# Performance work log

Hardware: AMD Instinct MI355X
Metric: run time of the kernel (lower is better)

## Reference

```python
import jax, jax.numpy as jnp
import numpy as np
from functools import lru_cache
from jax.scipy.linalg import expm

N_QUBITS = 6
DIM = 2 ** N_QUBITS          # 64
N_PAULI = 4 ** N_QUBITS      # 4096


@lru_cache(maxsize=None)
def _pauli_tensor_np(n_qubits):
    # All n-qubit Pauli strings as dense matrices, ordered base-4
    # (digit 0..3 -> I, X, Y, Z; most-significant digit = first qubit).
    I = np.eye(2, dtype=np.complex64)
    X = np.array([[0, 1], [1, 0]], dtype=np.complex64)
    Y = np.array([[0, -1j], [1j, 0]], dtype=np.complex64)
    Z = np.array([[1, 0], [0, -1]], dtype=np.complex64)
    base = np.stack([I, X, Y, Z])  # [4,2,2]
    T = base
    for _ in range(n_qubits - 1):
        k, d = T.shape[0], T.shape[1]
        T = np.einsum('iab,jcd->ijacbd', T, base).reshape(k * 4, d * 2, d * 2)
    return np.ascontiguousarray(T.astype(np.complex64))  # [4^n, 2^n, 2^n]


def setup_inputs() -> dict:
    key = jax.random.key(0)
    kx, kw, kb = jax.random.split(key, 3)
    x = jax.random.normal(kx, (512, 4000), dtype=jnp.float32)
    weight = jax.random.normal(kw, (4, N_PAULI - 1), dtype=jnp.float32)
    bias = jax.random.normal(kb, (DIM,), dtype=jnp.float32)
    return {"x": x, "weight": weight, "bias": bias}


def reference(x, weight, bias):
    # x: [B, in_dim] float32; weight: [n_reps, 4^n - 1]; bias: [out_dim]
    B, in_dim = x.shape
    n_reps = weight.shape[0]
    out_dim = bias.shape[0]
    P = jnp.asarray(_pauli_tensor_np(N_QUBITS))  # [4096, 64, 64] complex64

    # Pad data coefficients up to the full Pauli basis (identity included).
    xp = jnp.pad(x, ((0, 0), (0, N_PAULI - in_dim))).astype(jnp.complex64)

    # Data-encoding Hamiltonian per sample: H_d[b] = sum_p x[b,p] * P[p]
    Hd = jnp.einsum('bp,pij->bij', xp, P)                       # [B,64,64]
    Ud = jax.vmap(expm)(-1j * Hd)                               # [B,64,64]

    # Trainable Hamiltonians per rep (identity Pauli excluded -> global phase).
    Hp = jnp.einsum('rp,pij->rij', weight.astype(jnp.complex64), P[1:])
    Up = jax.vmap(expm)(-1j * Hp)                               # [R,64,64]

    # Data re-uploading circuit on |0...0>: repeat (U_param @ U_data).
    psi = jnp.zeros((B, DIM), dtype=jnp.complex64).at[:, 0].set(1.0)
    for r in range(n_reps):
        psi = jnp.einsum('bij,bj->bi', Ud, psi)
        psi = jnp.einsum('ij,bj->bi', Up[r], psi)

    # Observables are computational-basis projectors |k><k|, k < out_dim:
    # <psi|O_k|psi> = |psi_k|^2
    probs = (psi[:, :out_dim].real ** 2 + psi[:, :out_dim].imag ** 2)
    return probs.astype(jnp.float32) + bias
```

## Files before the change

### kernel.cpp

```cpp
#include <hip/hip_runtime.h>
#include <math.h>

typedef float2 cplx;
typedef __attribute__((ext_vector_type(8))) short short8v;
typedef __attribute__((ext_vector_type(4))) short short4v;
typedef __attribute__((ext_vector_type(4))) float float4v;

#define TPB 256
#define IN_DIM 4000
#define NREPS 4

#define C0f  1.0f
#define C1f  1.0f
#define C2f  0.5f
#define C3f  0.16666667f
#define C4f  0.041666668f
#define C5f  8.3333333e-3f
#define C6f  1.3888889e-3f
#define C7f  1.9841270e-4f
#define C8f  2.4801587e-5f
#define C9f  2.7557319e-6f
#define C10f 2.7557319e-7f
#define C11f 2.5052108e-8f
#define C12f 2.0876757e-9f
#define C13f 1.6059044e-10f
#define C14f 1.1470746e-11f
#define C15f 7.6471637e-13f

#define MFMA(A,B,C) __builtin_amdgcn_mfma_f32_16x16x32_bf16((A),(B),(C),0,0,0)


__device__ __forceinline__ int idxSw(int a, int b) {
    return (a << 6) + ((((b >> 3) + a) & 7) << 3) + (b & 7);
}
__device__ __forceinline__ short f2bf(float f) {
    unsigned u = __float_as_uint(f);
    return (short)((u + 0x7FFF + ((u >> 16) & 1)) >> 16);
}
__device__ __forceinline__ float bf2f(short s) {
    return __uint_as_float(((unsigned)(unsigned short)s) << 16);
}
__device__ __forceinline__ short8v neg8(short8v a) {
    int4 u; __builtin_memcpy(&u, &a, 16);
    u.x ^= 0x80008000; u.y ^= 0x80008000; u.z ^= 0x80008000; u.w ^= 0x80008000;
    short8v r; __builtin_memcpy(&r, &u, 16); return r;
}

template<int AM, int BM>
__device__ __forceinline__ void mm_mfma(const short* __restrict__ As,
                                        const short* __restrict__ Bs,
                                        int li, int q, int mh, int nh,
                                        float4v* __restrict__ accR,
                                        float4v* __restrict__ accI)
{
    #pragma unroll
    for (int ks = 0; ks < 2; ks++) {
        const int ch = ks * 4 + q;
        short8v arh[2], arl[2], cRh[2], cRl[2], cIh[2], cIl[2];
        #pragma unroll
        for (int dm = 0; dm < 2; dm++) {
            int r = ((mh * 2 + dm) << 4) + li;
            int off = (r << 6) + (((ch + r) & 7) << 3);
            arh[dm] = *(const short8v*)(As + off);
            arl[dm] = *(const short8v*)(As + 4096 + off);
            short8v aih = *(const short8v*)(As + 8192 + off);
            short8v ail = *(const short8v*)(As + 12288 + off);
            short8v nih = neg8(aih), nil_ = neg8(ail);
            cRh[dm] = (AM == 2) ? aih : nih;
            cRl[dm] = (AM == 2) ? ail : nil_;
            cIh[dm] = (AM == 2) ? nih : aih;
            cIl[dm] = (AM == 2) ? nil_ : ail;
        }
        #pragma unroll
        for (int dn = 0; dn < 2; dn++) {
            int n = ((nh * 2 + dn) << 4) + li;
            int off = (n << 6) + (((ch + n) & 7) << 3);
            short8v brh = *(const short8v*)(Bs + off);
            short8v brl = *(const short8v*)(Bs + 4096 + off);
            short8v bih = *(const short8v*)(Bs + 8192 + off);
            short8v bil = *(const short8v*)(Bs + 12288 + off);
            if (BM == 1) { brh = neg8(brh); brl = neg8(brl); }
            #pragma unroll
            for (int dm = 0; dm < 2; dm++) {
                int ti = dm * 2 + dn;
                accR[ti] = MFMA(arh[dm], brh, accR[ti]);
                accR[ti] = MFMA(arh[dm], brl, accR[ti]);
                accR[ti] = MFMA(arl[dm], brh, accR[ti]);
                accR[ti] = MFMA(cRh[dm], bih, accR[ti]);
                accR[ti] = MFMA(cRh[dm], bil, accR[ti]);
                accR[ti] = MFMA(cRl[dm], bih, accR[ti]);
                accI[ti] = MFMA(arh[dm], bih, accI[ti]);
                accI[ti] = MFMA(arh[dm], bil, accI[ti]);
                accI[ti] = MFMA(arl[dm], bih, accI[ti]);
                accI[ti] = MFMA(cIh[dm], brh, accI[ti]);
                accI[ti] = MFMA(cIh[dm], brl, accI[ti]);
                accI[ti] = MFMA(cIl[dm], brh, accI[ti]);
            }
        }
    }
}

__device__ __forceinline__ void write_row(short* __restrict__ S, int li, int q,
                                          int mh, int nh,
                                          const float4v* cre, const float4v* cim)
{
    #pragma unroll
    for (int dm = 0; dm < 2; dm++)
    #pragma unroll
    for (int dn = 0; dn < 2; dn++) {
        int ti = dm * 2 + dn;
        int c = ((nh * 2 + dn) << 4) + li;
        #pragma unroll
        for (int reg = 0; reg < 4; reg++) {
            int r = ((mh * 2 + dm) << 4) + q * 4 + reg;
            int off = idxSw(r, c);
            float vr = cre[ti][reg], vi = cim[ti][reg];
            short rh = f2bf(vr), rl = f2bf(vr - bf2f(rh));
            short ih = f2bf(vi), il = f2bf(vi - bf2f(ih));
            S[off] = rh; S[4096 + off] = rl; S[8192 + off] = ih; S[12288 + off] = il;
        }
    }
}

__device__ __forceinline__ void write_rowT(short* __restrict__ S, int li, int q,
                                           int mh, int nh,
                                           const float4v* cre, const float4v* cim)
{
    #pragma unroll
    for (int dm = 0; dm < 2; dm++)
    #pragma unroll
    for (int dn = 0; dn < 2; dn++) {
        int ti = dm * 2 + dn;
        int c = ((nh * 2 + dn) << 4) + li;
        int k0 = ((mh * 2 + dm) << 4) + q * 4;
        int off = idxSw(c, k0);
        short4v rh, rl, ih, il;
        #pragma unroll
        for (int reg = 0; reg < 4; reg++) {
            float vr = cre[ti][reg], vi = cim[ti][reg];
            short h1 = f2bf(vr); rh[reg] = h1; rl[reg] = f2bf(vr - bf2f(h1));
            short h2 = f2bf(vi); ih[reg] = h2; il[reg] = f2bf(vi - bf2f(h2));
        }
        *(short4v*)(S + off) = rh;
        *(short4v*)(S + 4096 + off) = rl;
        *(short4v*)(S + 8192 + off) = ih;
        *(short4v*)(S + 12288 + off) = il;
    }
}

__device__ __forceinline__ void gather_tile(const short* __restrict__ S, int li, int q,
                                            int mh, int nh, float4v* bre, float4v* bim)
{
    #pragma unroll
    for (int dm = 0; dm < 2; dm++)
    #pragma unroll
    for (int dn = 0; dn < 2; dn++) {
        int ti = dm * 2 + dn;
        int c = ((nh * 2 + dn) << 4) + li;
        #pragma unroll
        for (int reg = 0; reg < 4; reg++) {
            int r = ((mh * 2 + dm) << 4) + q * 4 + reg;
            int off = idxSw(r, c);
            bre[ti][reg] = bf2f(S[off]) + bf2f(S[4096 + off]);
            bim[ti][reg] = bf2f(S[8192 + off]) + bf2f(S[12288 + off]);
        }
    }
}

__device__ __forceinline__ void adddiag(float4v* ure, float cI, int li, int q, int mh, int nh)
{
    #pragma unroll
    for (int dm = 0; dm < 2; dm++)
    #pragma unroll
    for (int dn = 0; dn < 2; dn++) {
        if (2 * mh + dm == 2 * nh + dn) {
            #pragma unroll
            for (int e = 0; e < 4; e++)
                if (li == q * 4 + e) ure[dm * 2 + dn][e] += cI;
        }
    }
}

__device__ __forceinline__ void pauli_masks(int p, int& xm, int& zm) {
    xm = 0; zm = 0;
    #pragma unroll
    for (int k = 0; k < 6; k++) {
        int lo = (p >> (2 * k)) & 1;
        int hi = (p >> (2 * k + 1)) & 1;
        zm |= hi << k;
        xm |= (hi ^ lo) << k;
    }
}
__device__ __forceinline__ cplx pauli_phase(float v, int xm, int zm) {
    int ny = __popc(xm & zm) & 3;
    if (ny == 0) return make_float2(v, 0.f);
    if (ny == 1) return make_float2(0.f, -v);
    if (ny == 2) return make_float2(-v, 0.f);
    return make_float2(0.f, v);
}

__device__ __forceinline__ void expm_core(char* __restrict__ LDS,
                                          const float* __restrict__ src, bool isW,
                                          int t, float4v* ure, float4v* uim)
{
    short* S0 = (short*)LDS;
    short* S1 = (short*)(LDS + 32768);
    cplx*  W  = (cplx*)(LDS + 32768);
    float* red = (float*)(LDS + 65536);
    const int lane = t & 63, wv = t >> 6;

    float sumsq = 0.f;
    #pragma unroll
    for (int n = 0; n < 16; n++) {
        int p = t + TPB * n;
        float v = isW ? ((p == 0) ? 0.f : src[p - 1])
                      : ((p < IN_DIM) ? src[p] : 0.f);
        sumsq += v * v;
        int xm, zm; pauli_masks(p, xm, zm);
        W[(xm << 6) + zm] = pauli_phase(v, xm, zm);
    }
    #pragma unroll
    for (int d = 32; d >= 1; d >>= 1) sumsq += __shfl_xor(sumsq, d, 64);
    if (lane == 0) red[wv] = sumsq;
    __syncthreads();

    float fro = sqrtf(64.f * (red[0] + red[1] + red[2] + red[3]));
    int s1 = 0; { float nn = fro; while (nn > 8.f && s1 < 24) { nn *= 0.5f; s1++; } }
    float sc1 = exp2f((float)(-s1));

    cplx hv[16];
    #pragma unroll
    for (int rr = 0; rr < 16; rr++) hv[rr] = W[(((wv << 4) + rr) << 6) + lane];
    #pragma unroll
    for (int d = 1; d < 64; d <<= 1) {
        float sg = (lane & d) ? -1.f : 1.f;
        #pragma unroll
        for (int rr = 0; rr < 16; rr++) {
            float px = __shfl_xor(hv[rr].x, d, 64);
            float py = __shfl_xor(hv[rr].y, d, 64);
            hv[rr].x = fmaf(sg, hv[rr].x, px);
            hv[rr].y = fmaf(sg, hv[rr].y, py);
        }
    }
    __syncthreads();

    #pragma unroll
    for (int rr = 0; rr < 16; rr++) {
        int m = (wv << 4) + rr;
        int c = lane ^ m;
        float vr = hv[rr].y * sc1, vi = -hv[rr].x * sc1;
        short rh = f2bf(vr), rl = f2bf(vr - bf2f(rh));
        short ih = f2bf(vi), il = f2bf(vi - bf2f(ih));
        int off = idxSw(lane, c);
        S0[off] = rh; S0[4096 + off] = rl; S0[8192 + off] = ih; S0[12288 + off] = il;
    }
    __syncthreads();

    const int li = lane & 15, q = lane >> 4;
    const int mh = wv & 1, nh = wv >> 1;
    const float4v z4 = {0.f, 0.f, 0.f, 0.f};
    float4v accR[4], accI[4];
    #define ZERO_ACC _Pragma("unroll") for (int i2 = 0; i2 < 4; i2++) { accR[i2]=z4; accI[i2]=z4; }

    ZERO_ACC
    mm_mfma<0, 1>(S0, S0, li, q, mh, nh, accR, accI);
    float ss = 0.f;
    #pragma unroll
    for (int ti = 0; ti < 4; ti++)
        #pragma unroll
        for (int e = 0; e < 4; e++)
            ss += accR[ti][e]*accR[ti][e] + accI[ti][e]*accI[ti][e];
    #pragma unroll
    for (int d = 32; d >= 1; d >>= 1) ss += __shfl_xor(ss, d, 64);
    if (lane == 0) red[4 + wv] = ss;
    __syncthreads();

    float bound = sqrtf(sqrtf(red[4] + red[5] + red[6] + red[7]));
    int ds = 0; { float nn = bound; while (nn > 3.4f && ds < 12) { nn *= 0.5f; ds++; } }
    const int s = s1 + ds;
    float dsc = exp2f((float)(-ds)), dsc2 = dsc * dsc;

    float4v bre[4], bim[4];
    gather_tile(S0, li, q, mh, nh, bre, bim);

    #pragma unroll
    for (int ti = 0; ti < 4; ti++) { ure[ti] = accR[ti] * dsc2; uim[ti] = accI[ti] * dsc2; }
    write_rowT(S1, li, q, mh, nh, ure, uim);
    __syncthreads();

    {
        float ca = C15f * dsc;
        #pragma unroll
        for (int ti = 0; ti < 4; ti++) { ure[ti] = ca * bre[ti]; uim[ti] = ca * bim[ti]; }
        adddiag(ure, C14f, li, q, mh, nh);
        write_rowT(S0, li, q, mh, nh, ure, uim);
    }
    __syncthreads();

    const float cIc[7] = { C0f, C2f, C4f, C6f, C8f, C10f, C12f };
    const float cAc[7] = { C1f, C3f, C5f, C7f, C9f, C11f, C13f };
    for (int j = 6; j >= 0; j--) {
        ZERO_ACC
        mm_mfma<2, 0>(S1, S0, li, q, mh, nh, accR, accI);
        __syncthreads();
        float ca = cAc[j] * dsc, cI = cIc[j];
        #pragma unroll
        for (int ti = 0; ti < 4; ti++) {
            ure[ti] = accR[ti] + ca * bre[ti];
            uim[ti] = accI[ti] + ca * bim[ti];
        }
        adddiag(ure, cI, li, q, mh, nh);
        write_rowT(S0, li, q, mh, nh, ure, uim);
        __syncthreads();
    }

    for (int sq = 0; sq < s; sq++) {
        write_row(S1, li, q, mh, nh, ure, uim);
        if (sq > 0) write_rowT(S0, li, q, mh, nh, ure, uim);
        __syncthreads();
        ZERO_ACC
        mm_mfma<0, 0>(S1, S0, li, q, mh, nh, accR, accI);
        __syncthreads();
        #pragma unroll
        for (int ti = 0; ti < 4; ti++) { ure[ti] = accR[ti]; uim[ti] = accI[ti]; }
    }
    #undef ZERO_ACC
}

__device__ __forceinline__ cplx matvec_partial(const cplx* __restrict__ M,
                                               const cplx* __restrict__ pin,
                                               int i, int g)
{
    float ax = 0.f, ay = 0.f;
    const float4* Mr = (const float4*)(M + (i << 6));
    #pragma unroll
    for (int c = 0; c < 4; c++) {
        int ch = ((g << 2) + c + (i & 15)) & 15;
        int b = (ch >> 2) & 1;
        float4 m01 = Mr[(ch << 1) + b];
        float4 m23 = Mr[(ch << 1) + 1 - b];
        const cplx* p = pin + (ch << 2);
        cplx p0 = p[0], p1 = p[1], p2 = p[2], p3 = p[3];
        ax = fmaf(m01.x, p0.x, fmaf(-m01.y, p0.y, ax));
        ay = fmaf(m01.x, p0.y, fmaf( m01.y, p0.x, ay));
        ax = fmaf(m01.z, p1.x, fmaf(-m01.w, p1.y, ax));
        ay = fmaf(m01.z, p1.y, fmaf( m01.w, p1.x, ay));
        ax = fmaf(m23.x, p2.x, fmaf(-m23.y, p2.y, ax));
        ay = fmaf(m23.x, p2.y, fmaf( m23.y, p2.x, ay));
        ax = fmaf(m23.z, p3.x, fmaf(-m23.w, p3.y, ax));
        ay = fmaf(m23.z, p3.y, fmaf( m23.w, p3.x, ay));
    }
    return make_float2(ax, ay);
}

__global__ __launch_bounds__(TPB) void up_kernel(const float* __restrict__ w,
                                                 cplx* __restrict__ ws)
{
    __shared__ float4 LDSf4[4290];
    char* LDS = (char*)LDSf4;
    const int t = threadIdx.x, r = blockIdx.x;
    float4v ure[4], uim[4];
    expm_core(LDS, w + (size_t)r * 4095, true, t, ure, uim);

    const int lane = t & 63, wv = t >> 6, li = lane & 15, q = lane >> 4;
    const int mh = wv & 1, nh = wv >> 1;
    cplx* dst = ws + ((size_t)r << 12);
    #pragma unroll
    for (int dm = 0; dm < 2; dm++)
    #pragma unroll
    for (int dn = 0; dn < 2; dn++) {
        int ti = dm * 2 + dn;
        int c = ((nh * 2 + dn) << 4) + li;
        int cs = c ^ (((c >> 4) & 1) << 1);
        #pragma unroll
        for (int reg = 0; reg < 4; reg++) {
            int rr = ((mh * 2 + dm) << 4) + q * 4 + reg;
            dst[(rr << 6) + cs] = make_float2(ure[ti][reg], uim[ti][reg]);
        }
    }
}

__global__ __launch_bounds__(TPB) void circuit_kernel(const float* __restrict__ x,
                                                      const cplx* __restrict__ ws,
                                                      const float* __restrict__ bias,
                                                      float* __restrict__ out)
{
    __shared__ float4 LDSf4[4290];
    char* LDS = (char*)LDSf4;
    const int t = threadIdx.x, b = blockIdx.x;
    float4v ure[4], uim[4];
    expm_core(LDS, x + (size_t)b * IN_DIM, false, t, ure, uim);

    cplx* Ud   = (cplx*)(LDS + 32768);
    cplx* UpS  = (cplx*)LDS;
    cplx* psiA = (cplx*)(LDS + 65568);
    cplx* psiB = (cplx*)(LDS + 66080);
    cplx* part = (cplx*)(LDS + 66592);

    const int lane = t & 63, wv = t >> 6, li = lane & 15, q = lane >> 4;
    const int mh = wv & 1, nh = wv >> 1;
    #pragma unroll
    for (int dm = 0; dm < 2; dm++)
    #pragma unroll
    for (int dn = 0; dn < 2; dn++) {
        int ti = dm * 2 + dn;
        int c = ((nh * 2 + dn) << 4) + li;
        int cs = c ^ (((c >> 4) & 1) << 1);
        #pragma unroll
        for (int reg = 0; reg < 4; reg++) {
            int rr = ((mh * 2 + dm) << 4) + q * 4 + reg;
            Ud[(rr << 6) + cs] = make_float2(ure[ti][reg], uim[ti][reg]);
        }
    }
    if (t < 64) psiA[t] = make_float2(t == 0 ? 1.f : 0.f, 0.f);
    __syncthreads();

    const int i = t & 63, g = t >> 6;
    for (int r = 0; r < NREPS; r++) {
        const float4* srcv = (const float4*)(ws + ((size_t)r << 12));
        float4* dstY = (float4*)UpS;
        #pragma unroll
        for (int n = 0; n < 8; n++) dstY[n * TPB + t] = srcv[n * TPB + t];
        __syncthreads();
        part[t] = matvec_partial(Ud, psiA, i, g);
        __syncthreads();
        if (t < 64) {
            cplx a0 = part[t], a1 = part[64 + t], a2 = part[128 + t], a3 = part[192 + t];
            psiB[t] = make_float2(a0.x + a1.x + a2.x + a3.x, a0.y + a1.y + a2.y + a3.y);
        }
        __syncthreads();
        part[t] = matvec_partial(UpS, psiB, i, g);
        __syncthreads();
        if (t < 64) {
            cplx a0 = part[t], a1 = part[64 + t], a2 = part[128 + t], a3 = part[192 + t];
            psiA[t] = make_float2(a0.x + a1.x + a2.x + a3.x, a0.y + a1.y + a2.y + a3.y);
        }
        __syncthreads();
    }
    if (t < 64) {
        cplx pv = psiA[t];
        out[(b << 6) + t] = fmaf(pv.x, pv.x, fmaf(pv.y, pv.y, bias[t]));
    }
}

extern "C" void kernel_launch(void* const* d_in, const int* in_sizes, int n_in,
                              void* d_out, int out_size, void* d_ws, size_t ws_size,
                              hipStream_t stream)
{
    const float* x    = (const float*)d_in[0];
    const float* w    = (const float*)d_in[1];
    const float* bias = (const float*)d_in[2];
    float* out = (float*)d_out;
    cplx* ws   = (cplx*)d_ws;

    int B = in_sizes[0] / IN_DIM;

    hipLaunchKernelGGL(up_kernel,      dim3(NREPS), dim3(TPB), 0, stream, w, ws);
    hipLaunchKernelGGL(circuit_kernel, dim3(B),     dim3(TPB), 0, stream, x, ws, bias, out);
}
```

Before: 166.1 us.

## Template expm core on wave count; use 1024-thread up_kernel and wave-local matvec

Makes the expm routine a template over waves per block, so up_kernel runs with 16 waves (one 16x16 tile per wave) instead of 4, shortening the serial critical path of the 4-block parameter expm. The circuit matvec now has each wave own 16 rows and reduce with shuffles instead of an LDS partial-sum pass, which removes a barrier and a reduction step per half-rep. Pauli mask computation is hoisted out of the load loop and one barrier after the Walsh transform is dropped. Using 1024 threads raises per-block register pressure and barrier cost in up_kernel.

```diff
diff --git a/kernel.cpp b/kernel.cpp
--- a/kernel.cpp
+++ b/kernel.cpp
@@ -6,7 +6,6 @@
 typedef __attribute__((ext_vector_type(4))) short short4v;
 typedef __attribute__((ext_vector_type(4))) float float4v;
 
-#define TPB 256
 #define IN_DIM 4000
 #define NREPS 4
 
@@ -46,20 +45,20 @@
     short8v r; __builtin_memcpy(&r, &u, 16); return r;
 }
 
-template<int AM, int BM>
+template<int AM, int BM, int ND>
 __device__ __forceinline__ void mm_mfma(const short* __restrict__ As,
                                         const short* __restrict__ Bs,
-                                        int li, int q, int mh, int nh,
+                                        int li, int q, int mb, int nb,
                                         float4v* __restrict__ accR,
                                         float4v* __restrict__ accI)
 {
     #pragma unroll
     for (int ks = 0; ks < 2; ks++) {
         const int ch = ks * 4 + q;
-        short8v arh[2], arl[2], cRh[2], cRl[2], cIh[2], cIl[2];
-        #pragma unroll
-        for (int dm = 0; dm < 2; dm++) {
-            int r = ((mh * 2 + dm) << 4) + li;
+        short8v arh[ND], arl[ND], cRh[ND], cRl[ND], cIh[ND], cIl[ND];
+        #pragma unroll
+        for (int dm = 0; dm < ND; dm++) {
+            int r = ((mb + dm) << 4) + li;
             int off = (r << 6) + (((ch + r) & 7) << 3);
             arh[dm] = *(const short8v*)(As + off);
             arl[dm] = *(const short8v*)(As + 4096 + off);
@@ -72,8 +71,8 @@
             cIl[dm] = (AM == 2) ? nil_ : ail;
         }
         #pragma unroll
-        for (int dn = 0; dn < 2; dn++) {
-            int n = ((nh * 2 + dn) << 4) + li;
+        for (int dn = 0; dn < ND; dn++) {
+            int n = ((nb + dn) << 4) + li;
             int off = (n << 6) + (((ch + n) & 7) << 3);
             short8v brh = *(const short8v*)(Bs + off);
             short8v brl = *(const short8v*)(Bs + 4096 + off);
@@ -81,8 +80,8 @@
             short8v bil = *(const short8v*)(Bs + 12288 + off);
             if (BM == 1) { brh = neg8(brh); brl = neg8(brl); }
             #pragma unroll
-            for (int dm = 0; dm < 2; dm++) {
-                int ti = dm * 2 + dn;
+            for (int dm = 0; dm < ND; dm++) {
+                int ti = dm * ND + dn;
                 accR[ti] = MFMA(arh[dm], brh, accR[ti]);
                 accR[ti] = MFMA(arh[dm], brl, accR[ti]);
                 accR[ti] = MFMA(arl[dm], brh, accR[ti]);
@@ -100,19 +99,20 @@
     }
 }
 
+template<int ND>
 __device__ __forceinline__ void write_row(short* __restrict__ S, int li, int q,
-                                          int mh, int nh,
+                                          int mb, int nb,
                                           const float4v* cre, const float4v* cim)
 {
     #pragma unroll
-    for (int dm = 0; dm < 2; dm++)
-    #pragma unroll
-    for (int dn = 0; dn < 2; dn++) {
-        int ti = dm * 2 + dn;
-        int c = ((nh * 2 + dn) << 4) + li;
+    for (int dm = 0; dm < ND; dm++)
+    #pragma unroll
+    for (int dn = 0; dn < ND; dn++) {
+        int ti = dm * ND + dn;
+        int c = ((nb + dn) << 4) + li;
         #pragma unroll
         for (int reg = 0; reg < 4; reg++) {
-            int r = ((mh * 2 + dm) << 4) + q * 4 + reg;
+            int r = ((mb + dm) << 4) + q * 4 + reg;
             int off = idxSw(r, c);
             float vr = cre[ti][reg], vi = cim[ti][reg];
             short rh = f2bf(vr), rl = f2bf(vr - bf2f(rh));
@@ -122,17 +122,18 @@
     }
 }
 
+template<int ND>
 __device__ __forceinline__ void write_rowT(short* __restrict__ S, int li, int q,
-                                           int mh, int nh,
+                                           int mb, int nb,
                                            const float4v* cre, const float4v* cim)
 {
     #pragma unroll
-    for (int dm = 0; dm < 2; dm++)
-    #pragma unroll
-    for (int dn = 0; dn < 2; dn++) {
-        int ti = dm * 2 + dn;
-        int c = ((nh * 2 + dn) << 4) + li;
-        int k0 = ((mh * 2 + dm) << 4) + q * 4;
+    for (int dm = 0; dm < ND; dm++)
+    #pragma unroll
+    for (int dn = 0; dn < ND; dn++) {
+        int ti = dm * ND + dn;
+        int c = ((nb + dn) << 4) + li;
+        int k0 = ((mb + dm) << 4) + q * 4;
         int off = idxSw(c, k0);
         short4v rh, rl, ih, il;
         #pragma unroll
@@ -148,18 +149,19 @@
     }
 }
 
+template<int ND>
 __device__ __forceinline__ void gather_tile(const short* __restrict__ S, int li, int q,
-                                            int mh, int nh, float4v* bre, float4v* bim)
-{
-    #pragma unroll
-    for (int dm = 0; dm < 2; dm++)
-    #pragma unroll
-    for (int dn = 0; dn < 2; dn++) {
-        int ti = dm * 2 + dn;
-        int c = ((nh * 2 + dn) << 4) + li;
+                                            int mb, int nb, float4v* bre, float4v* bim)
+{
+    #pragma unroll
+    for (int dm = 0; dm < ND; dm++)
+    #pragma unroll
+    for (int dn = 0; dn < ND; dn++) {
+        int ti = dm * ND + dn;
+        int c = ((nb + dn) << 4) + li;
         #pragma unroll
         for (int reg = 0; reg < 4; reg++) {
-            int r = ((mh * 2 + dm) << 4) + q * 4 + reg;
+            int r = ((mb + dm) << 4) + q * 4 + reg;
             int off = idxSw(r, c);
             bre[ti][reg] = bf2f(S[off]) + bf2f(S[4096 + off]);
             bim[ti][reg] = bf2f(S[8192 + off]) + bf2f(S[12288 + off]);
@@ -167,30 +169,41 @@
     }
 }
 
-__device__ __forceinline__ void adddiag(float4v* ure, float cI, int li, int q, int mh, int nh)
-{
-    #pragma unroll
-    for (int dm = 0; dm < 2; dm++)
-    #pragma unroll
-    for (int dn = 0; dn < 2; dn++) {
-        if (2 * mh + dm == 2 * nh + dn) {
+template<int ND>
+__device__ __forceinline__ void adddiag(float4v* u, float cI, int li, int q, int mb, int nb)
+{
+    #pragma unroll
+    for (int dm = 0; dm < ND; dm++)
+    #pragma unroll
+    for (int dn = 0; dn < ND; dn++) {
+        if (mb + dm == nb + dn) {
             #pragma unroll
             for (int e = 0; e < 4; e++)
-                if (li == q * 4 + e) ure[dm * 2 + dn][e] += cI;
-        }
-    }
-}
-
-__device__ __forceinline__ void pauli_masks(int p, int& xm, int& zm) {
-    xm = 0; zm = 0;
-    #pragma unroll
-    for (int k = 0; k < 6; k++) {
-        int lo = (p >> (2 * k)) & 1;
-        int hi = (p >> (2 * k + 1)) & 1;
-        zm |= hi << k;
-        xm |= (hi ^ lo) << k;
-    }
-}
+                if (li == q * 4 + e) u[dm * ND + dn][e] += cI;
+        }
+    }
+}
+
+template<int ND>
+__device__ __forceinline__ void store_tiles(cplx* __restrict__ dst, int li, int q,
+                                            int mb, int nb,
+                                            const float4v* ure, const float4v* uim)
+{
+    #pragma unroll
+    for (int dm = 0; dm < ND; dm++)
+    #pragma unroll
+    for (int dn = 0; dn < ND; dn++) {
+        int ti = dm * ND + dn;
+        int c = ((nb + dn) << 4) + li;
+        int cs = c ^ (((c >> 4) & 1) << 1);
+        #pragma unroll
+        for (int reg = 0; reg < 4; reg++) {
+            int r = ((mb + dm) << 4) + q * 4 + reg;
+            dst[(r << 6) + cs] = make_float2(ure[ti][reg], uim[ti][reg]);
+        }
+    }
+}
+
 __device__ __forceinline__ cplx pauli_phase(float v, int xm, int zm) {
     int ny = __popc(xm & zm) & 3;
     if (ny == 0) return make_float2(v, 0.f);
@@ -199,24 +212,42 @@
     return make_float2(0.f, v);
 }
 
+template<int WPB>
 __device__ __forceinline__ void expm_core(char* __restrict__ LDS,
                                           const float* __restrict__ src, bool isW,
                                           int t, float4v* ure, float4v* uim)
 {
+    constexpr int ND    = (WPB == 4) ? 2 : 1;
+    constexpr int NT    = ND * ND;
+    constexpr int TPBv  = WPB * 64;
+    constexpr int LITER = 4096 / TPBv;
+    constexpr int ROWS  = 64 / WPB;
+    constexpr int L4    = (WPB == 4) ? 4 : 5;
     short* S0 = (short*)LDS;
     short* S1 = (short*)(LDS + 32768);
     cplx*  W  = (cplx*)(LDS + 32768);
     float* red = (float*)(LDS + 65536);
     const int lane = t & 63, wv = t >> 6;
-
+    const int li = lane & 15, q = lane >> 4;
+    const int mb = (WPB == 4) ? ((wv & 1) << 1) : (wv & 3);
+    const int nb = (WPB == 4) ? ((wv >> 1) << 1) : (wv >> 2);
+
+    int xmt = 0, zmt = 0;
+    #pragma unroll
+    for (int k = 0; k < 6; k++) {
+        int lo = (t >> (2 * k)) & 1, hi = (t >> (2 * k + 1)) & 1;
+        zmt |= hi << k; xmt |= (hi ^ lo) << k;
+    }
     float sumsq = 0.f;
     #pragma unroll
-    for (int n = 0; n < 16; n++) {
-        int p = t + TPB * n;
+    for (int n = 0; n < LITER; n++) {
+        int p = t + TPBv * n;
+        int lo0 = n & 1, hi0 = (n >> 1) & 1, lo1 = (n >> 2) & 1, hi1 = (n >> 3) & 1;
+        int zmn = hi0 | (hi1 << 1), xmn = (hi0 ^ lo0) | ((hi1 ^ lo1) << 1);
+        int xm = xmt | (xmn << L4), zm = zmt | (zmn << L4);
         float v = isW ? ((p == 0) ? 0.f : src[p - 1])
                       : ((p < IN_DIM) ? src[p] : 0.f);
         sumsq += v * v;
-        int xm, zm; pauli_masks(p, xm, zm);
         W[(xm << 6) + zm] = pauli_phase(v, xm, zm);
     }
     #pragma unroll
@@ -224,29 +255,31 @@
     if (lane == 0) red[wv] = sumsq;
     __syncthreads();
 
-    float fro = sqrtf(64.f * (red[0] + red[1] + red[2] + red[3]));
+    float rs = 0.f;
+    #pragma unroll
+    for (int i2 = 0; i2 < WPB; i2++) rs += red[i2];
+    float fro = sqrtf(64.f * rs);
     int s1 = 0; { float nn = fro; while (nn > 8.f && s1 < 24) { nn *= 0.5f; s1++; } }
     float sc1 = exp2f((float)(-s1));
 
-    cplx hv[16];
-    #pragma unroll
-    for (int rr = 0; rr < 16; rr++) hv[rr] = W[(((wv << 4) + rr) << 6) + lane];
+    cplx hv[ROWS];
+    #pragma unroll
+    for (int rr = 0; rr < ROWS; rr++) hv[rr] = W[((wv * ROWS + rr) << 6) + lane];
     #pragma unroll
     for (int d = 1; d < 64; d <<= 1) {
         float sg = (lane & d) ? -1.f : 1.f;
         #pragma unroll
-        for (int rr = 0; rr < 16; rr++) {
+        for (int rr = 0; rr < ROWS; rr++) {
             float px = __shfl_xor(hv[rr].x, d, 64);
             float py = __shfl_xor(hv[rr].y, d, 64);
             hv[rr].x = fmaf(sg, hv[rr].x, px);
             hv[rr].y = fmaf(sg, hv[rr].y, py);
         }
     }
-    __syncthreads();
-
-    #pragma unroll
-    for (int rr = 0; rr < 16; rr++) {
-        int m = (wv << 4) + rr;
+
+    #pragma unroll
+    for (int rr = 0; rr < ROWS; rr++) {
+        int m = wv * ROWS + rr;
         int c = lane ^ m;
         float vr = hv[rr].y * sc1, vi = -hv[rr].x * sc1;
         short rh = f2bf(vr), rl = f2bf(vr - bf2f(rh));
@@ -256,44 +289,45 @@
     }
     __syncthreads();
 
-    const int li = lane & 15, q = lane >> 4;
-    const int mh = wv & 1, nh = wv >> 1;
     const float4v z4 = {0.f, 0.f, 0.f, 0.f};
-    float4v accR[4], accI[4];
-    #define ZERO_ACC _Pragma("unroll") for (int i2 = 0; i2 < 4; i2++) { accR[i2]=z4; accI[i2]=z4; }
+    float4v accR[NT], accI[NT];
+    #define ZERO_ACC _Pragma("unroll") for (int i2 = 0; i2 < NT; i2++) { accR[i2]=z4; accI[i2]=z4; }
 
     ZERO_ACC
-    mm_mfma<0, 1>(S0, S0, li, q, mh, nh, accR, accI);
+    mm_mfma<0, 1, ND>(S0, S0, li, q, mb, nb, accR, accI);
     float ss = 0.f;
     #pragma unroll
-    for (int ti = 0; ti < 4; ti++)
+    for (int ti = 0; ti < NT; ti++)
         #pragma unroll
         for (int e = 0; e < 4; e++)
             ss += accR[ti][e]*accR[ti][e] + accI[ti][e]*accI[ti][e];
     #pragma unroll
     for (int d = 32; d >= 1; d >>= 1) ss += __shfl_xor(ss, d, 64);
-    if (lane == 0) red[4 + wv] = ss;
-    __syncthreads();
-
-    float bound = sqrtf(sqrtf(red[4] + red[5] + red[6] + red[7]));
+    if (lane == 0) red[WPB + wv] = ss;
+    __syncthreads();
+
+    rs = 0.f;
+    #pragma unroll
+    for (int i2 = 0; i2 < WPB; i2++) rs += red[WPB + i2];
+    float bound = sqrtf(sqrtf(rs));
     int ds = 0; { float nn = bound; while (nn > 3.4f && ds < 12) { nn *= 0.5f; ds++; } }
     const int s = s1 + ds;
     float dsc = exp2f((float)(-ds)), dsc2 = dsc * dsc;
 
-    float4v bre[4], bim[4];
-    gather_tile(S0, li, q, mh, nh, bre, bim);
-
-    #pragma unroll
-    for (int ti = 0; ti < 4; ti++) { ure[ti] = accR[ti] * dsc2; uim[ti] = accI[ti] * dsc2; }
-    write_rowT(S1, li, q, mh, nh, ure, uim);
+    float4v bre[NT], bim[NT];
+    gather_tile<ND>(S0, li, q, mb, nb, bre, bim);
+
+    #pragma unroll
+    for (int ti = 0; ti < NT; ti++) { ure[ti] = accR[ti] * dsc2; uim[ti] = accI[ti] * dsc2; }
+    write_rowT<ND>(S1, li, q, mb, nb, ure, uim);
     __syncthreads();
 
     {
         float ca = C15f * dsc;
         #pragma unroll
-        for (int ti = 0; ti < 4; ti++) { ure[ti] = ca * bre[ti]; uim[ti] = ca * bim[ti]; }
-        adddiag(ure, C14f, li, q, mh, nh);
-        write_rowT(S0, li, q, mh, nh, ure, uim);
+        for (int ti = 0; ti < NT; ti++) { ure[ti] = ca * bre[ti]; uim[ti] = ca * bim[ti]; }
+        adddiag<ND>(ure, C14f, li, q, mb, nb);
+        write_rowT<ND>(S0, li, q, mb, nb, ure, uim);
     }
     __syncthreads();
 
@@ -301,41 +335,43 @@
     const float cAc[7] = { C1f, C3f, C5f, C7f, C9f, C11f, C13f };
     for (int j = 6; j >= 0; j--) {
         ZERO_ACC
-        mm_mfma<2, 0>(S1, S0, li, q, mh, nh, accR, accI);
+        mm_mfma<2, 0, ND>(S1, S0, li, q, mb, nb, accR, accI);
         __syncthreads();
         float ca = cAc[j] * dsc, cI = cIc[j];
         #pragma unroll
-        for (int ti = 0; ti < 4; ti++) {
+        for (int ti = 0; ti < NT; ti++) {
             ure[ti] = accR[ti] + ca * bre[ti];
             uim[ti] = accI[ti] + ca * bim[ti];
         }
-        adddiag(ure, cI, li, q, mh, nh);
-        write_rowT(S0, li, q, mh, nh, ure, uim);
+        adddiag<ND>(ure, cI, li, q, mb, nb);
+        write_rowT<ND>(S0, li, q, mb, nb, ure, uim);
         __syncthreads();
     }
 
     for (int sq = 0; sq < s; sq++) {
-        write_row(S1, li, q, mh, nh, ure, uim);
-        if (sq > 0) write_rowT(S0, li, q, mh, nh, ure, uim);
+        write_row<ND>(S1, li, q, mb, nb, ure, uim);
+        if (sq > 0) write_rowT<ND>(S0, li, q, mb, nb, ure, uim);
         __syncthreads();
         ZERO_ACC
-        mm_mfma<0, 0>(S1, S0, li, q, mh, nh, accR, accI);
-        __syncthreads();
-        #pragma unroll
-        for (int ti = 0; ti < 4; ti++) { ure[ti] = accR[ti]; uim[ti] = accI[ti]; }
+        mm_mfma<0, 0, ND>(S1, S0, li, q, mb, nb, accR, accI);
+        __syncthreads();
+        #pragma unroll
+        for (int ti = 0; ti < NT; ti++) { ure[ti] = accR[ti]; uim[ti] = accI[ti]; }
     }
     #undef ZERO_ACC
 }
 
-__device__ __forceinline__ cplx matvec_partial(const cplx* __restrict__ M,
-                                               const cplx* __restrict__ pin,
-                                               int i, int g)
-{
+__device__ __forceinline__ cplx matvec_wave(const cplx* __restrict__ M,
+                                            const cplx* __restrict__ pin,
+                                            int lane, int wv)
+{
+    const int rr = (wv << 4) + (lane & 15);
+    const int kc = lane >> 4;
     float ax = 0.f, ay = 0.f;
-    const float4* Mr = (const float4*)(M + (i << 6));
+    const float4* Mr = (const float4*)(M + (rr << 6));
     #pragma unroll
     for (int c = 0; c < 4; c++) {
-        int ch = ((g << 2) + c + (i & 15)) & 15;
+        int ch = ((kc << 2) + c + rr) & 15;
         int b = (ch >> 2) & 1;
         float4 m01 = Mr[(ch << 1) + b];
         float4 m23 = Mr[(ch << 1) + 1 - b];
@@ -350,91 +386,58 @@
         ax = fmaf(m23.z, p3.x, fmaf(-m23.w, p3.y, ax));
         ay = fmaf(m23.z, p3.y, fmaf( m23.w, p3.x, ay));
     }
+    ax += __shfl_xor(ax, 16, 64); ay += __shfl_xor(ay, 16, 64);
+    ax += __shfl_xor(ax, 32, 64); ay += __shfl_xor(ay, 32, 64);
     return make_float2(ax, ay);
 }
 
-__global__ __launch_bounds__(TPB) void up_kernel(const float* __restrict__ w,
-                                                 cplx* __restrict__ ws)
-{
-    __shared__ float4 LDSf4[4290];
+__global__ __launch_bounds__(1024) void up_kernel(const float* __restrict__ w,
+                                                  cplx* __restrict__ ws)
+{
+    __shared__ float4 LDSf4[4104];
     char* LDS = (char*)LDSf4;
     const int t = threadIdx.x, r = blockIdx.x;
-    float4v ure[4], uim[4];
-    expm_core(LDS, w + (size_t)r * 4095, true, t, ure, uim);
+    float4v ure[1], uim[1];
+    expm_core<16>(LDS, w + (size_t)r * 4095, true, t, ure, uim);
 
     const int lane = t & 63, wv = t >> 6, li = lane & 15, q = lane >> 4;
-    const int mh = wv & 1, nh = wv >> 1;
-    cplx* dst = ws + ((size_t)r << 12);
-    #pragma unroll
-    for (int dm = 0; dm < 2; dm++)
-    #pragma unroll
-    for (int dn = 0; dn < 2; dn++) {
-        int ti = dm * 2 + dn;
-        int c = ((nh * 2 + dn) << 4) + li;
-        int cs = c ^ (((c >> 4) & 1) << 1);
-        #pragma unroll
-        for (int reg = 0; reg < 4; reg++) {
-            int rr = ((mh * 2 + dm) << 4) + q * 4 + reg;
-            dst[(rr << 6) + cs] = make_float2(ure[ti][reg], uim[ti][reg]);
-        }
-    }
-}
-
-__global__ __launch_bounds__(TPB) void circuit_kernel(const float* __restrict__ x,
+    store_tiles<1>(ws + ((size_t)r << 12), li, q, wv & 3, wv >> 2, ure, uim);
+}
+
+__global__ __launch_bounds__(256) void circuit_kernel(const float* __restrict__ x,
                                                       const cplx* __restrict__ ws,
                                                       const float* __restrict__ bias,
                                                       float* __restrict__ out)
 {
-    __shared__ float4 LDSf4[4290];
+    __shared__ float4 LDSf4[4168];
     char* LDS = (char*)LDSf4;
     const int t = threadIdx.x, b = blockIdx.x;
     float4v ure[4], uim[4];
-    expm_core(LDS, x + (size_t)b * IN_DIM, false, t, ure, uim);
+    expm_core<4>(LDS, x + (size_t)b * IN_DIM, false, t, ure, uim);
 
     cplx* Ud   = (cplx*)(LDS + 32768);
     cplx* UpS  = (cplx*)LDS;
-    cplx* psiA = (cplx*)(LDS + 65568);
-    cplx* psiB = (cplx*)(LDS + 66080);
-    cplx* part = (cplx*)(LDS + 66592);
+    cplx* psiA = (cplx*)(LDS + 65664);
+    cplx* psiB = (cplx*)(LDS + 66176);
 
     const int lane = t & 63, wv = t >> 6, li = lane & 15, q = lane >> 4;
-    const int mh = wv & 1, nh = wv >> 1;
-    #pragma unroll
-    for (int dm = 0; dm < 2; dm++)
-    #pragma unroll
-    for (int dn = 0; dn < 2; dn++) {
-        int ti = dm * 2 + dn;
-        int c = ((nh * 2 + dn) << 4) + li;
-        int cs = c ^ (((c >> 4) & 1) << 1);
-        #pragma unroll
-        for (int reg = 0; reg < 4; reg++) {
-            int rr = ((mh * 2 + dm) << 4) + q * 4 + reg;
-            Ud[(rr << 6) + cs] = make_float2(ure[ti][reg], uim[ti][reg]);
-        }
-    }
+    store_tiles<2>(Ud, li, q, (wv & 1) << 1, (wv >> 1) << 1, ure, uim);
     if (t < 64) psiA[t] = make_float2(t == 0 ? 1.f : 0.f, 0.f);
     __syncthreads();
 
-    const int i = t & 63, g = t >> 6;
+    const int rowi = (wv << 4) + (lane & 15);
     for (int r = 0; r < NREPS; r++) {
-        const float4* srcv = (const float4*)(ws + ((size_t)r << 12));
-        float4* dstY = (float4*)UpS;
-        #pragma unroll
-        for (int n = 0; n < 8; n++) dstY[n * TPB + t] = srcv[n * TPB + t];
-        __syncthreads();
-        part[t] = matvec_partial(Ud, psiA, i, g);
-        __syncthreads();
-        if (t < 64) {
-            cplx a0 = part[t], a1 = part[64 + t], a2 = part[128 + t], a3 = part[192 + t];
-            psiB[t] = make_float2(a0.x + a1.x + a2.x + a3.x, a0.y + a1.y + a2.y + a3.y);
-        }
-        __syncthreads();
-        part[t] = matvec_partial(UpS, psiB, i, g);
-        __syncthreads();
-        if (t < 64) {
-            cplx a0 = part[t], a1 = part[64 + t], a2 = part[128 + t], a3 = part[192 + t];
-            psiA[t] = make_float2(a0.x + a1.x + a2.x + a3.x, a0.y + a1.y + a2.y + a3.y);
-        }
+        {
+            const float4* srcv = (const float4*)(ws + ((size_t)r << 12));
+            float4* dstY = (float4*)UpS;
+            #pragma unroll
+            for (int n = 0; n < 8; n++) dstY[n * 256 + t] = srcv[n * 256 + t];
+        }
+        cplx v1 = matvec_wave(Ud, psiA, lane, wv);
+        if (lane < 16) psiB[rowi] = v1;
+        __syncthreads();
+        cplx v2 = matvec_wave(UpS, psiB, lane, wv);
+        if (lane < 16) psiA[rowi] = v2;
         __syncthreads();
     }
     if (t < 64) {
@@ -455,6 +458,6 @@
 
     int B = in_sizes[0] / IN_DIM;
 
-    hipLaunchKernelGGL(up_kernel,      dim3(NREPS), dim3(TPB), 0, stream, w, ws);
-    hipLaunchKernelGGL(circuit_kernel, dim3(B),     dim3(TPB), 0, stream, x, ws, bias, out);
-}
+    hipLaunchKernelGGL(up_kernel,      dim3(NREPS), dim3(1024), 0, stream, w, ws);
+    hipLaunchKernelGGL(circuit_kernel, dim3(B),     dim3(256),  0, stream, x, ws, bias, out);
+}
```

Result: faster. 155.1 us (-6.7%).
